# Performance work log

Measured on AMD Instinct MI355X. Metric: run time of the kernel, lower is better.

The kernel has to match this reference:

```python
import jax, jax.numpy as jnp
import numpy as np

B, N, D = 2, 2048, 768
H = 12
HD = D // H  # 64

def setup_inputs() -> dict:
    key = jax.random.key(0)
    ks = jax.random.split(key, 5)
    scale = 1.0 / np.sqrt(D)
    return {
        "x": jax.random.normal(ks[0], (B, N, D), dtype=jnp.float32),
        "W_kqv": jax.random.normal(ks[1], (H, 3 * HD, D), dtype=jnp.float32) * scale,
        "b_kqv": jax.random.normal(ks[2], (H, 3 * HD), dtype=jnp.float32) * 0.01,
        "W_proj": jax.random.normal(ks[3], (D, D), dtype=jnp.float32) * scale,
        "b_proj": jax.random.normal(ks[4], (D,), dtype=jnp.float32) * 0.01,
    }

def reference(x, W_kqv, b_kqv, W_proj, b_proj):
    # Per-head Linear: x @ W_h^T + b_h, all heads at once -> [B, H, N, 3*HD]
    kqv = jnp.einsum('bnd,hod->bhno', x, W_kqv) + b_kqv[None, :, None, :]
    k, q, v = jnp.split(kqv, 3, axis=-1)  # each [B, H, N, HD]
    # scores = q @ k^T / sqrt(head_dim)  (attention_scores(a=k, b=q))
    scores = jnp.einsum('bhqd,bhkd->bhqk', q, k) / jnp.sqrt(jnp.asarray(HD, x.dtype))
    # causal mask (tril): masked_fill with -inf where mask == 0
    causal = jnp.tril(jnp.ones((N, N), dtype=bool))
    scores = jnp.where(causal[None, None, :, :], scores, -jnp.inf)
    attn = jax.nn.softmax(scores, axis=-1)
    sa = jnp.einsum('bhqk,bhkd->bhqd', attn, v)  # [B, H, N, HD]
    # concat heads along feature dim (head order preserved)
    sa = sa.transpose(0, 2, 1, 3).reshape(B, N, D)
    # output projection
    return sa @ W_proj.T + b_proj
```

## Files before the change

### kernel.cpp

```cpp
#include <hip/hip_runtime.h>

#define BB 2
#define SEQ 2048
#define DIM 768
#define NH 12
#define HD 64

typedef _Float16 half8 __attribute__((ext_vector_type(8)));
typedef float floatx4 __attribute__((ext_vector_type(4)));

__device__ __forceinline__ int fragL(int kb, int r) { return (kb << 4) | ((r ^ kb) & 15); }

__device__ __forceinline__ void cvt_store8(_Float16* dst, float4 a, float4 b) {
    half8 h;
    h[0] = (_Float16)a.x; h[1] = (_Float16)a.y; h[2] = (_Float16)a.z; h[3] = (_Float16)a.w;
    h[4] = (_Float16)b.x; h[5] = (_Float16)b.y; h[6] = (_Float16)b.z; h[7] = (_Float16)b.w;
    *(half8*)dst = h;
}

__device__ __forceinline__ void gl_lds16(const _Float16* g, _Float16* l) {
    __builtin_amdgcn_global_load_lds(
        (const __attribute__((address_space(1))) void*)g,
        (__attribute__((address_space(3))) void*)l, 16, 0, 0);
}

__global__ __launch_bounds__(256)
void kqv_gemm(const float* __restrict__ x, const float* __restrict__ Wk,
              const float* __restrict__ bias, _Float16* __restrict__ kb,
              _Float16* __restrict__ qb, _Float16* __restrict__ vb) {
    __shared__ _Float16 Asl[8 * 64 * 8];
    __shared__ _Float16 Bsl[4 * 64 * 8];
    const int t = threadIdx.x;
    const int w = t >> 6, lane = t & 63, quad = lane >> 4, l15 = lane & 15;
    const int m0 = blockIdx.y * 128, c0 = blockIdx.x * 64;

    const floatx4 z4 = {0.f, 0.f, 0.f, 0.f};
    floatx4 acc[2][4];
    #pragma unroll
    for (int i = 0; i < 2; ++i)
        #pragma unroll
        for (int j = 0; j < 4; ++j) acc[i][j] = z4;

    const int ar = t >> 1, akb = (t & 1) * 2;
    const int amt = ar >> 4, arr = ar & 15;
    const int br = t >> 2, bkb = t & 3;
    const int bnt = br >> 4, brr = br & 15;
    const int rdL = fragL(quad, l15);
    _Float16* aw0 = &Asl[((amt << 6) + fragL(akb,     arr)) * 8];
    _Float16* aw1 = &Asl[((amt << 6) + fragL(akb + 1, arr)) * 8];
    _Float16* bw0 = &Bsl[((bnt << 6) + fragL(bkb,     brr)) * 8];

    const float* pax = x  + (size_t)(m0 + ar) * DIM + (t & 1) * 16;
    const float* pbw = Wk + (size_t)(c0 + br) * DIM + (t & 3) * 8;

    for (int k0 = 0; k0 < DIM; k0 += 32) {
        float4 a0 = *(const float4*)(pax + k0);
        float4 a1 = *(const float4*)(pax + k0 + 4);
        float4 a2 = *(const float4*)(pax + k0 + 8);
        float4 a3 = *(const float4*)(pax + k0 + 12);
        float4 b0 = *(const float4*)(pbw + k0);
        float4 b1 = *(const float4*)(pbw + k0 + 4);
        __syncthreads();
        cvt_store8(aw0, a0, a1);
        cvt_store8(aw1, a2, a3);
        cvt_store8(bw0, b0, b1);
        __syncthreads();
        half8 af0 = *(const half8*)&Asl[(((w * 2 + 0) << 6) + rdL) * 8];
        half8 af1 = *(const half8*)&Asl[(((w * 2 + 1) << 6) + rdL) * 8];
        #pragma unroll
        for (int j = 0; j < 4; ++j) {
            half8 bf = *(const half8*)&Bsl[((j << 6) + rdL) * 8];
            acc[0][j] = __builtin_amdgcn_mfma_f32_16x16x32_f16(af0, bf, acc[0][j], 0, 0, 0);
            acc[1][j] = __builtin_amdgcn_mfma_f32_16x16x32_f16(af1, bf, acc[1][j], 0, 0, 0);
        }
    }

    #pragma unroll
    for (int j = 0; j < 4; ++j) {
        const int cbase = c0 + j * 16;
        const int h = cbase / 192;
        const int rem = cbase - h * 192;
        const int part = rem >> 6;
        const int d = (rem & 63) + l15;
        _Float16* dst = (part == 0) ? kb : (part == 1 ? qb : vb);
        const float bv = bias[cbase + l15];
        #pragma unroll
        for (int i = 0; i < 2; ++i)
            #pragma unroll
            for (int r = 0; r < 4; ++r) {
                const int m = m0 + w * 32 + i * 16 + quad * 4 + r;
                const int bidx = m >> 11, n = m & (SEQ - 1);
                dst[(((size_t)(bidx * NH + h) * SEQ + n) << 6) + d] =
                    (_Float16)(acc[i][j][r] + bv);
            }
    }
}

__global__ __launch_bounds__(256)
void v_transpose(const _Float16* __restrict__ vb, _Float16* __restrict__ vbT) {
    __shared__ _Float16 T[64 * 72];
    const int t = threadIdx.x;
    const int s0 = blockIdx.x * 64;
    const size_t base = (size_t)blockIdx.y * (SEQ * HD);
    {
        const int s = t >> 2, doff = (t & 3) * 16;
        const _Float16* src = vb + base + (size_t)(s0 + s) * HD + doff;
        *(half8*)&T[s * 72 + doff]     = *(const half8*)src;
        *(half8*)&T[s * 72 + doff + 8] = *(const half8*)(src + 8);
    }
    __syncthreads();
    {
        const int d = t >> 2, soff = (t & 3) * 16;
        half8 o0, o1;
        #pragma unroll
        for (int k = 0; k < 8; ++k) o0[k] = T[(soff + k) * 72 + d];
        #pragma unroll
        for (int k = 0; k < 8; ++k) o1[k] = T[(soff + 8 + k) * 72 + d];
        _Float16* dst = vbT + base + (size_t)d * SEQ + s0 + soff;
        *(half8*)dst       = o0;
        *(half8*)(dst + 8) = o1;
    }
}

__global__ __launch_bounds__(256)
void attn_mfma(const _Float16* __restrict__ qb, const _Float16* __restrict__ kbuf,
               const _Float16* __restrict__ vbT, _Float16* __restrict__ sa) {
    __shared__ _Float16 Kl[2][64 * 64];
    __shared__ _Float16 Vl[2][64 * 64];
    __shared__ _Float16 Pl[4][16 * 72];
    const int qt = blockIdx.x, bh = blockIdx.y;
    const int t = threadIdx.x, w = t >> 6, lane = t & 63, quad = lane >> 4, l15 = lane & 15;
    const size_t base = (size_t)bh * (SEQ * HD);
    const int i0 = qt * 64 + w * 16;
    _Float16* Pw = Pl[w];
    const _Float16* Kg = kbuf + base;
    const _Float16* Vg = vbT + base;

    const int lr = lane >> 3, gg = lane & 7;
    const int gs = (gg ^ (lr & 7)) * 8;

    half8 aq[2];
    aq[0] = *(const half8*)(qb + base + (size_t)(i0 + l15) * HD + quad * 8);
    aq[1] = *(const half8*)(qb + base + (size_t)(i0 + l15) * HD + 32 + quad * 8);
    #pragma unroll
    for (int k = 0; k < 8; ++k) {
        aq[0][k] = aq[0][k] * (_Float16)0.125f;
        aq[1][k] = aq[1][k] * (_Float16)0.125f;
    }

    const floatx4 z4 = {0.f, 0.f, 0.f, 0.f};
    floatx4 O[4];
    #pragma unroll
    for (int dt = 0; dt < 4; ++dt) O[dt] = z4;
    float l_part[4] = {0.f, 0.f, 0.f, 0.f};

    #pragma unroll
    for (int p = 0; p < 2; ++p) {
        const int c = w * 2 + p, row = c * 8 + lr;
        gl_lds16(Kg + (size_t)row * HD + gs,  &Kl[0][c * 512]);
        gl_lds16(Vg + (size_t)row * SEQ + gs, &Vl[0][c * 512]);
    }

    const int swz = l15 & 7;

    for (int kt = 0; kt <= qt; ++kt) {
        const int buf = kt & 1;
        const int j0 = kt * 64;
        __syncthreads();

        if (kt < qt) {
            const _Float16* Kn = Kg + (size_t)(j0 + 64) * HD;
            const _Float16* Vn = Vg + (j0 + 64);
            #pragma unroll
            for (int p = 0; p < 2; ++p) {
                const int c = w * 2 + p, row = c * 8 + lr;
                gl_lds16(Kn + (size_t)row * HD + gs,  &Kl[buf ^ 1][c * 512]);
                gl_lds16(Vn + (size_t)row * SEQ + gs, &Vl[buf ^ 1][c * 512]);
            }
        }

        floatx4 S[4];
        #pragma unroll
        for (int nt = 0; nt < 4; ++nt) S[nt] = z4;
        #pragma unroll
        for (int ks = 0; ks < 2; ++ks)
            #pragma unroll
            for (int nt = 0; nt < 4; ++nt) {
                half8 bk = *(const half8*)&Kl[buf][(nt * 16 + l15) * 64 +
                                                   (((ks * 4 + quad) ^ swz) << 3)];
                S[nt] = __builtin_amdgcn_mfma_f32_16x16x32_f16(aq[ks], bk, S[nt], 0, 0, 0);
            }

        const bool diag = (kt == qt);
        asm volatile("" ::: "memory");
        #pragma unroll
        for (int nt = 0; nt < 4; ++nt) {
            const int j = j0 + nt * 16 + l15;
            #pragma unroll
            for (int r = 0; r < 4; ++r) {
                float p = __expf(S[nt][r]);
                if (diag && j > (i0 + quad * 4 + r)) p = 0.f;
                l_part[r] += p;
                Pw[(quad * 4 + r) * 72 + nt * 16 + l15] = (_Float16)p;
            }
        }
        asm volatile("" ::: "memory");
        #pragma unroll
        for (int ks = 0; ks < 2; ++ks) {
            half8 ap = *(const half8*)&Pw[l15 * 72 + ks * 32 + quad * 8];
            #pragma unroll
            for (int dt = 0; dt < 4; ++dt) {
                half8 bv = *(const half8*)&Vl[buf][(dt * 16 + l15) * 64 +
                                                    (((ks * 4 + quad) ^ swz) << 3)];
                O[dt] = __builtin_amdgcn_mfma_f32_16x16x32_f16(ap, bv, O[dt], 0, 0, 0);
            }
        }
    }

    const int bidx = bh / NH, h = bh - bidx * NH;
    #pragma unroll
    for (int r = 0; r < 4; ++r) {
        float rs = l_part[r];
        #pragma unroll
        for (int off = 1; off < 16; off <<= 1) rs += __shfl_xor(rs, off);
        const float inv = 1.0f / rs;
        const int i = i0 + quad * 4 + r;
        #pragma unroll
        for (int dt = 0; dt < 4; ++dt)
            sa[(size_t)(bidx * SEQ + i) * DIM + h * HD + dt * 16 + l15] =
                (_Float16)(O[dt][r] * inv);
    }
}

__global__ __launch_bounds__(256)
void proj_gemm(const _Float16* __restrict__ A, const float* __restrict__ W,
               const float* __restrict__ bias, float* __restrict__ out) {
    __shared__ _Float16 Asl[8 * 64 * 8];
    __shared__ _Float16 Bsl[4 * 64 * 8];
    const int t = threadIdx.x;
    const int w = t >> 6, lane = t & 63, quad = lane >> 4, l15 = lane & 15;
    const int m0 = blockIdx.y * 128, c0 = blockIdx.x * 64;

    const floatx4 z4 = {0.f, 0.f, 0.f, 0.f};
    floatx4 acc[2][4];
    #pragma unroll
    for (int i = 0; i < 2; ++i)
        #pragma unroll
        for (int j = 0; j < 4; ++j) acc[i][j] = z4;

    const int ar = t >> 1, akb = (t & 1) * 2;
    const int amt = ar >> 4, arr = ar & 15;
    const int br = t >> 2, bkb = t & 3;
    const int bnt = br >> 4, brr = br & 15;
    const int rdL = fragL(quad, l15);
    _Float16* aw0 = &Asl[((amt << 6) + fragL(akb,     arr)) * 8];
    _Float16* aw1 = &Asl[((amt << 6) + fragL(akb + 1, arr)) * 8];
    _Float16* bw0 = &Bsl[((bnt << 6) + fragL(bkb,     brr)) * 8];

    const _Float16* pa = A + (size_t)(m0 + ar) * DIM + (t & 1) * 16;
    const float*    pb = W + (size_t)(c0 + br) * DIM + (t & 3) * 8;

    for (int k0 = 0; k0 < DIM; k0 += 32) {
        half8 h0 = *(const half8*)(pa + k0);
        half8 h1 = *(const half8*)(pa + k0 + 8);
        float4 b0 = *(const float4*)(pb + k0);
        float4 b1 = *(const float4*)(pb + k0 + 4);
        __syncthreads();
        *(half8*)aw0 = h0;
        *(half8*)aw1 = h1;
        cvt_store8(bw0, b0, b1);
        __syncthreads();
        half8 af0 = *(const half8*)&Asl[(((w * 2 + 0) << 6) + rdL) * 8];
        half8 af1 = *(const half8*)&Asl[(((w * 2 + 1) << 6) + rdL) * 8];
        #pragma unroll
        for (int j = 0; j < 4; ++j) {
            half8 bf = *(const half8*)&Bsl[((j << 6) + rdL) * 8];
            acc[0][j] = __builtin_amdgcn_mfma_f32_16x16x32_f16(af0, bf, acc[0][j], 0, 0, 0);
            acc[1][j] = __builtin_amdgcn_mfma_f32_16x16x32_f16(af1, bf, acc[1][j], 0, 0, 0);
        }
    }

    #pragma unroll
    for (int j = 0; j < 4; ++j) {
        const int cbase = c0 + j * 16;
        const float bv = bias[cbase + l15];
        #pragma unroll
        for (int i = 0; i < 2; ++i)
            #pragma unroll
            for (int r = 0; r < 4; ++r) {
                const int m = m0 + w * 32 + i * 16 + quad * 4 + r;
                out[(size_t)m * DIM + cbase + l15] = acc[i][j][r] + bv;
            }
    }
}

extern "C" void kernel_launch(void* const* d_in, const int* in_sizes, int n_in,
                              void* d_out, int out_size, void* d_ws, size_t ws_size,
                              hipStream_t stream) {
    (void)in_sizes; (void)n_in; (void)out_size; (void)ws_size;
    const float* x  = (const float*)d_in[0];
    const float* Wk = (const float*)d_in[1];
    const float* bk = (const float*)d_in[2];
    const float* Wp = (const float*)d_in[3];
    const float* bp = (const float*)d_in[4];
    float* out = (float*)d_out;

    _Float16* ws = (_Float16*)d_ws;
    const size_t per = (size_t)BB * NH * SEQ * HD;
    _Float16* kb  = ws;
    _Float16* qb  = ws + per;
    _Float16* vb  = ws + 2 * per;
    _Float16* vbT = ws + 3 * per;
    _Float16* sa  = ws + 4 * per;

    kqv_gemm  <<<dim3(36, 32), 256, 0, stream>>>(x, Wk, bk, kb, qb, vb);
    v_transpose<<<dim3(32, 24), 256, 0, stream>>>(vb, vbT);
    attn_mfma <<<dim3(32, 24), 256, 0, stream>>>(qb, kb, vbT, sa);
    proj_gemm <<<dim3(12, 32), 256, 0, stream>>>(sa, Wp, bp, out);
}
```

Before: 194.6 us.

## Pre-convert inputs to fp16 and use 128x128 LDS-DMA GEMM tiles

A new conversion kernel casts x, W_kqv and W_proj to fp16 in workspace. Both GEMMs are then rebuilt around a shared 128x128 tile core that loads straight into LDS with global_load_lds and runs a 4x4 MFMA grid per wave. This is meant to cut per-tile conversion work, raise data reuse and use direct-to-LDS transfers. In exchange it adds one launch, an extra global pass over the inputs, and fewer blocks per GEMM.

```diff
diff --git a/kernel.cpp b/kernel.cpp
--- a/kernel.cpp
+++ b/kernel.cpp
@@ -9,15 +9,6 @@
 typedef _Float16 half8 __attribute__((ext_vector_type(8)));
 typedef float floatx4 __attribute__((ext_vector_type(4)));
 
-__device__ __forceinline__ int fragL(int kb, int r) { return (kb << 4) | ((r ^ kb) & 15); }
-
-__device__ __forceinline__ void cvt_store8(_Float16* dst, float4 a, float4 b) {
-    half8 h;
-    h[0] = (_Float16)a.x; h[1] = (_Float16)a.y; h[2] = (_Float16)a.z; h[3] = (_Float16)a.w;
-    h[4] = (_Float16)b.x; h[5] = (_Float16)b.y; h[6] = (_Float16)b.z; h[7] = (_Float16)b.w;
-    *(half8*)dst = h;
-}
-
 __device__ __forceinline__ void gl_lds16(const _Float16* g, _Float16* l) {
     __builtin_amdgcn_global_load_lds(
         (const __attribute__((address_space(1))) void*)g,
@@ -25,59 +16,66 @@
 }
 
 __global__ __launch_bounds__(256)
-void kqv_gemm(const float* __restrict__ x, const float* __restrict__ Wk,
-              const float* __restrict__ bias, _Float16* __restrict__ kb,
-              _Float16* __restrict__ qb, _Float16* __restrict__ vb) {
-    __shared__ _Float16 Asl[8 * 64 * 8];
-    __shared__ _Float16 Bsl[4 * 64 * 8];
-    const int t = threadIdx.x;
-    const int w = t >> 6, lane = t & 63, quad = lane >> 4, l15 = lane & 15;
-    const int m0 = blockIdx.y * 128, c0 = blockIdx.x * 64;
-
-    const floatx4 z4 = {0.f, 0.f, 0.f, 0.f};
-    floatx4 acc[2][4];
-    #pragma unroll
-    for (int i = 0; i < 2; ++i)
-        #pragma unroll
-        for (int j = 0; j < 4; ++j) acc[i][j] = z4;
-
-    const int ar = t >> 1, akb = (t & 1) * 2;
-    const int amt = ar >> 4, arr = ar & 15;
-    const int br = t >> 2, bkb = t & 3;
-    const int bnt = br >> 4, brr = br & 15;
-    const int rdL = fragL(quad, l15);
-    _Float16* aw0 = &Asl[((amt << 6) + fragL(akb,     arr)) * 8];
-    _Float16* aw1 = &Asl[((amt << 6) + fragL(akb + 1, arr)) * 8];
-    _Float16* bw0 = &Bsl[((bnt << 6) + fragL(bkb,     brr)) * 8];
-
-    const float* pax = x  + (size_t)(m0 + ar) * DIM + (t & 1) * 16;
-    const float* pbw = Wk + (size_t)(c0 + br) * DIM + (t & 3) * 8;
-
-    for (int k0 = 0; k0 < DIM; k0 += 32) {
-        float4 a0 = *(const float4*)(pax + k0);
-        float4 a1 = *(const float4*)(pax + k0 + 4);
-        float4 a2 = *(const float4*)(pax + k0 + 8);
-        float4 a3 = *(const float4*)(pax + k0 + 12);
-        float4 b0 = *(const float4*)(pbw + k0);
-        float4 b1 = *(const float4*)(pbw + k0 + 4);
-        __syncthreads();
-        cvt_store8(aw0, a0, a1);
-        cvt_store8(aw1, a2, a3);
-        cvt_store8(bw0, b0, b1);
-        __syncthreads();
-        half8 af0 = *(const half8*)&Asl[(((w * 2 + 0) << 6) + rdL) * 8];
-        half8 af1 = *(const half8*)&Asl[(((w * 2 + 1) << 6) + rdL) * 8];
-        #pragma unroll
-        for (int j = 0; j < 4; ++j) {
-            half8 bf = *(const half8*)&Bsl[((j << 6) + rdL) * 8];
-            acc[0][j] = __builtin_amdgcn_mfma_f32_16x16x32_f16(af0, bf, acc[0][j], 0, 0, 0);
-            acc[1][j] = __builtin_amdgcn_mfma_f32_16x16x32_f16(af1, bf, acc[1][j], 0, 0, 0);
-        }
-    }
-
+void cvt3(const float* __restrict__ s0, _Float16* __restrict__ d0, int nb0,
+          const float* __restrict__ s1, _Float16* __restrict__ d1, int nb1,
+          const float* __restrict__ s2, _Float16* __restrict__ d2) {
+    int b = blockIdx.x;
+    const float* s; _Float16* d;
+    if (b < nb0)            { s = s0; d = d0; }
+    else if (b < nb0 + nb1) { s = s1; d = d1; b -= nb0; }
+    else                    { s = s2; d = d2; b -= nb0 + nb1; }
+    const int i = (b * 256 + threadIdx.x) * 8;
+    float4 a = *(const float4*)(s + i);
+    float4 c = *(const float4*)(s + i + 4);
+    half8 h;
+    h[0] = (_Float16)a.x; h[1] = (_Float16)a.y; h[2] = (_Float16)a.z; h[3] = (_Float16)a.w;
+    h[4] = (_Float16)c.x; h[5] = (_Float16)c.y; h[6] = (_Float16)c.z; h[7] = (_Float16)c.w;
+    *(half8*)(d + i) = h;
+}
+
+#define GEMM_CORE(ATYPE_PTR, BTYPE_PTR)                                         \
+    __shared__ _Float16 Asl[128 * 32];                                          \
+    __shared__ _Float16 Bsl[128 * 32];                                          \
+    const int t = threadIdx.x, w = t >> 6, lane = t & 63;                       \
+    const int quad = lane >> 4, l15 = lane & 15;                                \
+    const int wm = w >> 1, wn = w & 1;                                          \
+    const int m0 = blockIdx.y * 128, c0 = blockIdx.x * 128;                     \
+    const floatx4 z4 = {0.f, 0.f, 0.f, 0.f};                                    \
+    floatx4 acc[4][4];                                                          \
+    _Pragma("unroll") for (int i = 0; i < 4; ++i)                               \
+        _Pragma("unroll") for (int j = 0; j < 4; ++j) acc[i][j] = z4;           \
+    const _Float16* pA = ATYPE_PTR + (size_t)(m0 + w * 32 + l15) * DIM + quad * 8; \
+    const _Float16* pB = BTYPE_PTR + (size_t)(c0 + w * 32 + l15) * DIM + quad * 8; \
+    _Float16* ldsA0 = &Asl[(w * 2 + 0) * 512];                                  \
+    _Float16* ldsA1 = &Asl[(w * 2 + 1) * 512];                                  \
+    _Float16* ldsB0 = &Bsl[(w * 2 + 0) * 512];                                  \
+    _Float16* ldsB1 = &Bsl[(w * 2 + 1) * 512];                                  \
+    for (int k0 = 0; k0 < DIM; k0 += 32) {                                      \
+        __syncthreads();                                                        \
+        gl_lds16(pA + k0, ldsA0);                                               \
+        gl_lds16(pA + k0 + 16 * DIM, ldsA1);                                    \
+        gl_lds16(pB + k0, ldsB0);                                               \
+        gl_lds16(pB + k0 + 16 * DIM, ldsB1);                                    \
+        __syncthreads();                                                        \
+        half8 af[4], bf[4];                                                     \
+        _Pragma("unroll") for (int i = 0; i < 4; ++i)                           \
+            af[i] = *(const half8*)&Asl[(wm * 4 + i) * 512 + lane * 8];         \
+        _Pragma("unroll") for (int j = 0; j < 4; ++j)                           \
+            bf[j] = *(const half8*)&Bsl[(wn * 4 + j) * 512 + lane * 8];         \
+        _Pragma("unroll") for (int i = 0; i < 4; ++i)                           \
+            _Pragma("unroll") for (int j = 0; j < 4; ++j)                       \
+                acc[i][j] = __builtin_amdgcn_mfma_f32_16x16x32_f16(             \
+                    af[i], bf[j], acc[i][j], 0, 0, 0);                          \
+    }
+
+__global__ __launch_bounds__(256)
+void kqv_gemm2(const _Float16* __restrict__ xh, const _Float16* __restrict__ Wh,
+               const float* __restrict__ bias, _Float16* __restrict__ kb,
+               _Float16* __restrict__ qb, _Float16* __restrict__ vb) {
+    GEMM_CORE(xh, Wh)
     #pragma unroll
     for (int j = 0; j < 4; ++j) {
-        const int cbase = c0 + j * 16;
+        const int cbase = c0 + (wn * 4 + j) * 16;
         const int h = cbase / 192;
         const int rem = cbase - h * 192;
         const int part = rem >> 6;
@@ -85,13 +83,31 @@
         _Float16* dst = (part == 0) ? kb : (part == 1 ? qb : vb);
         const float bv = bias[cbase + l15];
         #pragma unroll
-        for (int i = 0; i < 2; ++i)
+        for (int i = 0; i < 4; ++i)
             #pragma unroll
             for (int r = 0; r < 4; ++r) {
-                const int m = m0 + w * 32 + i * 16 + quad * 4 + r;
+                const int m = m0 + (wm * 4 + i) * 16 + quad * 4 + r;
                 const int bidx = m >> 11, n = m & (SEQ - 1);
                 dst[(((size_t)(bidx * NH + h) * SEQ + n) << 6) + d] =
                     (_Float16)(acc[i][j][r] + bv);
+            }
+    }
+}
+
+__global__ __launch_bounds__(256)
+void proj_gemm2(const _Float16* __restrict__ A, const _Float16* __restrict__ Wh,
+                const float* __restrict__ bias, float* __restrict__ out) {
+    GEMM_CORE(A, Wh)
+    #pragma unroll
+    for (int j = 0; j < 4; ++j) {
+        const int cbase = c0 + (wn * 4 + j) * 16;
+        const float bv = bias[cbase + l15];
+        #pragma unroll
+        for (int i = 0; i < 4; ++i)
+            #pragma unroll
+            for (int r = 0; r < 4; ++r) {
+                const int m = m0 + (wm * 4 + i) * 16 + quad * 4 + r;
+                out[(size_t)m * DIM + cbase + l15] = acc[i][j][r] + bv;
             }
     }
 }
@@ -232,68 +248,6 @@
     }
 }
 
-__global__ __launch_bounds__(256)
-void proj_gemm(const _Float16* __restrict__ A, const float* __restrict__ W,
-               const float* __restrict__ bias, float* __restrict__ out) {
-    __shared__ _Float16 Asl[8 * 64 * 8];
-    __shared__ _Float16 Bsl[4 * 64 * 8];
-    const int t = threadIdx.x;
-    const int w = t >> 6, lane = t & 63, quad = lane >> 4, l15 = lane & 15;
-    const int m0 = blockIdx.y * 128, c0 = blockIdx.x * 64;
-
-    const floatx4 z4 = {0.f, 0.f, 0.f, 0.f};
-    floatx4 acc[2][4];
-    #pragma unroll
-    for (int i = 0; i < 2; ++i)
-        #pragma unroll
-        for (int j = 0; j < 4; ++j) acc[i][j] = z4;
-
-    const int ar = t >> 1, akb = (t & 1) * 2;
-    const int amt = ar >> 4, arr = ar & 15;
-    const int br = t >> 2, bkb = t & 3;
-    const int bnt = br >> 4, brr = br & 15;
-    const int rdL = fragL(quad, l15);
-    _Float16* aw0 = &Asl[((amt << 6) + fragL(akb,     arr)) * 8];
-    _Float16* aw1 = &Asl[((amt << 6) + fragL(akb + 1, arr)) * 8];
-    _Float16* bw0 = &Bsl[((bnt << 6) + fragL(bkb,     brr)) * 8];
-
-    const _Float16* pa = A + (size_t)(m0 + ar) * DIM + (t & 1) * 16;
-    const float*    pb = W + (size_t)(c0 + br) * DIM + (t & 3) * 8;
-
-    for (int k0 = 0; k0 < DIM; k0 += 32) {
-        half8 h0 = *(const half8*)(pa + k0);
-        half8 h1 = *(const half8*)(pa + k0 + 8);
-        float4 b0 = *(const float4*)(pb + k0);
-        float4 b1 = *(const float4*)(pb + k0 + 4);
-        __syncthreads();
-        *(half8*)aw0 = h0;
-        *(half8*)aw1 = h1;
-        cvt_store8(bw0, b0, b1);
-        __syncthreads();
-        half8 af0 = *(const half8*)&Asl[(((w * 2 + 0) << 6) + rdL) * 8];
-        half8 af1 = *(const half8*)&Asl[(((w * 2 + 1) << 6) + rdL) * 8];
-        #pragma unroll
-        for (int j = 0; j < 4; ++j) {
-            half8 bf = *(const half8*)&Bsl[((j << 6) + rdL) * 8];
-            acc[0][j] = __builtin_amdgcn_mfma_f32_16x16x32_f16(af0, bf, acc[0][j], 0, 0, 0);
-            acc[1][j] = __builtin_amdgcn_mfma_f32_16x16x32_f16(af1, bf, acc[1][j], 0, 0, 0);
-        }
-    }
-
-    #pragma unroll
-    for (int j = 0; j < 4; ++j) {
-        const int cbase = c0 + j * 16;
-        const float bv = bias[cbase + l15];
-        #pragma unroll
-        for (int i = 0; i < 2; ++i)
-            #pragma unroll
-            for (int r = 0; r < 4; ++r) {
-                const int m = m0 + w * 32 + i * 16 + quad * 4 + r;
-                out[(size_t)m * DIM + cbase + l15] = acc[i][j][r] + bv;
-            }
-    }
-}
-
 extern "C" void kernel_launch(void* const* d_in, const int* in_sizes, int n_in,
                               void* d_out, int out_size, void* d_ws, size_t ws_size,
                               hipStream_t stream) {
@@ -307,14 +261,23 @@
 
     _Float16* ws = (_Float16*)d_ws;
     const size_t per = (size_t)BB * NH * SEQ * HD;
+    const int nx = BB * SEQ * DIM;
+    const int nwk = NH * 3 * HD * DIM;
+    const int nwp = DIM * DIM;
     _Float16* kb  = ws;
     _Float16* qb  = ws + per;
     _Float16* vb  = ws + 2 * per;
     _Float16* vbT = ws + 3 * per;
     _Float16* sa  = ws + 4 * per;
-
-    kqv_gemm  <<<dim3(36, 32), 256, 0, stream>>>(x, Wk, bk, kb, qb, vb);
+    _Float16* xh  = ws + 5 * per;
+    _Float16* Wkh = xh + nx;
+    _Float16* Wph = Wkh + nwk;
+
+    const int nb0 = nx / 2048, nb1 = nwk / 2048, nb2 = nwp / 2048;
+    cvt3<<<dim3(nb0 + nb1 + nb2), 256, 0, stream>>>(x, xh, nb0, Wk, Wkh, nb1, Wp, Wph);
+
+    kqv_gemm2 <<<dim3(18, 32), 256, 0, stream>>>(xh, Wkh, bk, kb, qb, vb);
     v_transpose<<<dim3(32, 24), 256, 0, stream>>>(vb, vbT);
     attn_mfma <<<dim3(32, 24), 256, 0, stream>>>(qb, kb, vbT, sa);
-    proj_gemm <<<dim3(12, 32), 256, 0, stream>>>(sa, Wp, bp, out);
-}
+    proj_gemm2<<<dim3(6, 32), 256, 0, stream>>>(sa, Wph, bp, out);
+}
```

New measurement: 191.3 us. No clear change (-1.7%).
